# Kernel tuning notes

Hardware: AMD Instinct MI355X
Metric: run time of the kernel (lower is better)

Reference implementation:

```python
import jax, jax.numpy as jnp
import numpy as np
from jax import lax

SIGMA = 0.66  # e2cnn PointwiseAvgPoolAntialiased sigma -> 5x5 gaussian, stride 2, pad 2

def _conv(x, w, pad):
    return lax.conv_general_dilated(x, w, (1, 1), [(pad, pad), (pad, pad)],
                                    dimension_numbers=('NCHW', 'OIHW', 'NCHW'))

def _inner_bn(x, gamma, beta, fsize, eps=1e-5):
    # e2cnn InnerBatchNorm: stats shared across the fsize channels of each field
    B, C, H, W = x.shape
    F = C // fsize
    xr = x.reshape(B, F, fsize, H, W)
    m = xr.mean(axis=(0, 2, 3, 4), keepdims=True)
    v = xr.var(axis=(0, 2, 3, 4), keepdims=True)
    xr = (xr - m) * lax.rsqrt(v + eps)
    xr = xr * gamma.reshape(1, F, 1, 1, 1) + beta.reshape(1, F, 1, 1, 1)
    return xr.reshape(B, C, H, W)

def _gauss_pool(x):
    # antialiased avg-pool: depthwise 5x5 gaussian blur, stride 2, pad 2
    C = x.shape[1]
    r = jnp.arange(5.0) - 2.0
    k1 = jnp.exp(-r ** 2 / (2.0 * SIGMA ** 2))
    k2 = k1[:, None] * k1[None, :]
    k2 = (k2 / k2.sum()).astype(x.dtype)
    k = jnp.broadcast_to(k2, (C, 1, 5, 5))
    return lax.conv_general_dilated(x, k, (2, 2), [(2, 2), (2, 2)],
                                    feature_group_count=C,
                                    dimension_numbers=('NCHW', 'OIHW', 'NCHW'))

def _roi_align(feat, boxes, bidx, out=7, scale=0.25, ratio=2):
    # torchvision RoIAlign, aligned=True, sampling_ratio=2
    B, C, H, W = feat.shape
    Nb = boxes.shape[0]
    x1 = boxes[:, 0] * scale - 0.5
    y1 = boxes[:, 1] * scale - 0.5
    x2 = boxes[:, 2] * scale - 0.5
    y2 = boxes[:, 3] * scale - 0.5
    bw = (x2 - x1) / out
    bh = (y2 - y1) / out
    g = (jnp.arange(out * ratio, dtype=feat.dtype) + 0.5) / ratio  # [P] in bin units
    ys = y1[:, None] + bh[:, None] * g[None, :]  # [N,P]
    xs = x1[:, None] + bw[:, None] * g[None, :]
    vy = (ys >= -1.0) & (ys <= H)
    vx = (xs >= -1.0) & (xs <= W)
    y = jnp.clip(ys, 0.0, H - 1)
    x = jnp.clip(xs, 0.0, W - 1)
    y0f = jnp.floor(y); x0f = jnp.floor(x)
    y0 = y0f.astype(jnp.int32); x0 = x0f.astype(jnp.int32)
    yp = jnp.minimum(y0 + 1, H - 1); xp = jnp.minimum(x0 + 1, W - 1)
    ly = y - y0f; lx = x - x0f; hy = 1.0 - ly; hx = 1.0 - lx
    fp = feat.transpose(0, 2, 3, 1)  # [B,H,W,C]
    b3 = bidx[:, None, None]
    def gat(yi, xi):
        return fp[b3, yi[:, :, None], xi[:, None, :]]  # [N,P,P,C]
    val = (gat(y0, x0) * (hy[:, :, None] * hx[:, None, :])[..., None]
         + gat(y0, xp) * (hy[:, :, None] * lx[:, None, :])[..., None]
         + gat(yp, x0) * (ly[:, :, None] * hx[:, None, :])[..., None]
         + gat(yp, xp) * (ly[:, :, None] * lx[:, None, :])[..., None])
    val = val * (vy[:, :, None] & vx[:, None, :])[..., None].astype(val.dtype)
    val = val.reshape(Nb, out, ratio, out, ratio, C).mean(axis=(2, 4))
    return val.transpose(0, 3, 1, 2)  # [N,C,7,7]

def _gat_layer(x, src, dst, W, a_s, a_d, bias, heads, oc, concat, Nn):
    # PyG GATConv (eval mode: no dropout), negative_slope=0.2, self-loops in src/dst
    h = (x @ W.T).reshape(Nn, heads, oc)
    es = (h * a_s[None]).sum(-1)  # [N,H]
    ed = (h * a_d[None]).sum(-1)
    e = jax.nn.leaky_relu(es[src] + ed[dst], 0.2)  # [E,H]
    m = jax.ops.segment_max(e, dst, num_segments=Nn)
    e = jnp.exp(e - m[dst])
    den = jax.ops.segment_sum(e, dst, num_segments=Nn)
    alpha = e / (den[dst] + 1e-16)
    out = jax.ops.segment_sum(h[src] * alpha[..., None], dst, num_segments=Nn)
    out = out.reshape(Nn, heads * oc) if concat else out.mean(axis=1)
    return out + bias

def reference(images, boxes, box_batch_idx, edge_index,
              w_conv1, g1, b1, w_conv2, g2, b2, w_conv3, g3, b3,
              w_mlp1, b_mlp1, w_mlp2, b_mlp2,
              w_gat1, asrc1, adst1, bias1, w_gat2, asrc2, adst2, bias2,
              w_obj, b_obj, w_rel, b_rel):
    x = jax.nn.relu(_inner_bn(_conv(images, w_conv1, 1), g1, b1, 8))
    x = _gauss_pool(x)
    x = jax.nn.relu(_inner_bn(_conv(x, w_conv2, 1), g2, b2, 8))
    x = _gauss_pool(x)
    x = jax.nn.relu(_inner_bn(_conv(x, w_conv3, 0), g3, b3, 1))  # [B,64,56,56]
    roi = _roi_align(x, boxes, box_batch_idx)  # [N,64,7,7]
    Nn = roi.shape[0]
    r = roi.reshape(Nn, -1)
    h = jax.nn.relu(r @ w_mlp1.T + b_mlp1)
    h = jax.nn.relu(h @ w_mlp2.T + b_mlp2)
    loop = jnp.arange(Nn, dtype=edge_index.dtype)
    src = jnp.concatenate([edge_index[0], loop])
    dst = jnp.concatenate([edge_index[1], loop])
    h = _gat_layer(h, src, dst, w_gat1, asrc1, adst1, bias1, 4, 256, True, Nn)
    h = _gat_layer(h, src, dst, w_gat2, asrc2, adst2, bias2, 1, 256, False, Nn)
    obj_logits = h @ w_obj.T + b_obj
    ef = jnp.concatenate([h[edge_index[0]], h[edge_index[1]]], axis=1)
    rel_logits = ef @ w_rel.T + b_rel
    return obj_logits, rel_logits

def setup_inputs() -> dict:
    key = jax.random.key(0)
    ks = jax.random.split(key, 32)
    B, H, W = 4, 224, 224
    Nb, E, GH = 4096, 65536, 256
    images = jax.random.normal(ks[0], (B, 3, H, W), dtype=jnp.float32)
    x1 = jax.random.uniform(ks[1], (Nb,)) * 160.0
    y1 = jax.random.uniform(ks[2], (Nb,)) * 160.0
    bw = 16.0 + jax.random.uniform(ks[3], (Nb,)) * 48.0
    bh = 16.0 + jax.random.uniform(ks[4], (Nb,)) * 48.0
    boxes = jnp.stack([x1, y1, x1 + bw, y1 + bh], axis=1)
    box_batch_idx = jnp.sort(jax.random.randint(ks[5], (Nb,), 0, B, dtype=jnp.int32))
    edge_index = jax.random.randint(ks[6], (2, E), 0, Nb, dtype=jnp.int32)
    s = 0.02
    n = lambda k, shp: jax.random.normal(k, shp, dtype=jnp.float32) * s
    return {
        'images': images, 'boxes': boxes, 'box_batch_idx': box_batch_idx, 'edge_index': edge_index,
        'w_conv1': n(ks[7], (128, 3, 3, 3)), 'g1': jnp.ones((16,)), 'b1': jnp.zeros((16,)),
        'w_conv2': n(ks[8], (256, 128, 3, 3)), 'g2': jnp.ones((32,)), 'b2': jnp.zeros((32,)),
        'w_conv3': n(ks[9], (64, 256, 1, 1)), 'g3': jnp.ones((64,)), 'b3': jnp.zeros((64,)),
        'w_mlp1': n(ks[10], (GH, 64 * 7 * 7)), 'b_mlp1': jnp.zeros((GH,)),
        'w_mlp2': n(ks[11], (GH, GH)), 'b_mlp2': jnp.zeros((GH,)),
        'w_gat1': n(ks[12], (4 * GH, GH)), 'asrc1': n(ks[13], (4, GH)), 'adst1': n(ks[14], (4, GH)), 'bias1': jnp.zeros((4 * GH,)),
        'w_gat2': n(ks[15], (GH, 4 * GH)), 'asrc2': n(ks[16], (1, GH)), 'adst2': n(ks[17], (1, GH)), 'bias2': jnp.zeros((GH,)),
        'w_obj': n(ks[18], (151, GH)), 'b_obj': jnp.zeros((151,)),
        'w_rel': n(ks[19], (51, 2 * GH)), 'b_rel': jnp.zeros((51,)),
    }
```

## Files before the change

kernel.cpp:

```cpp
#include <hip/hip_runtime.h>
#include <hip/hip_bf16.h>
#include <cmath>

constexpr long Y1_F    = 0;
constexpr long Y3N_F   = 0;
constexpr long WM2B_F  = 0;
constexpr long WG1B_F  = 65536;
constexpr long WG2B_F  = 589824;
constexpr long ROI_F   = 12845056;
constexpr long Y2BF_F  = 12845056;
constexpr long WT2_F   = 16056320;
constexpr long O1_F    = 12845056;
constexpr long HG2_F   = 17039360;
constexpr long ES2_F   = 18087936;
constexpr long ED2_F   = 18092032;
constexpr long O2_F    = 18096128;
constexpr long Y2_F    = 25690112;
constexpr long HG1_F   = 25690112;
constexpr long ES1_F   = 29884416;
constexpr long ED1_F   = 29900800;
constexpr long Y4N_F   = 32112640;
constexpr long H1_F    = 32112640;
constexpr long H2_F    = 33161216;
constexpr long Y5N_F   = 35323904;
constexpr long STATS_F = 36126720;
constexpr long CNT_F   = 36127232;
constexpr long POS_F   = 36131328;
constexpr long OFF_F   = 36135424;
constexpr long EID_F   = 36139528;
constexpr long Y5T_F   = 36209160;
constexpr long WP_F    = 37011976;
constexpr long P1_F    = 37814792;
constexpr long P2_F    = 38023688;

struct GaussW { float w[25]; };

typedef __attribute__((ext_vector_type(8))) short bf16x8;
typedef __attribute__((ext_vector_type(4))) float f32x4;

static __device__ __forceinline__ unsigned short f2bf(float f) {
    unsigned int u = __float_as_uint(f);
    unsigned int r = (u + 0x7fffu + ((u >> 16) & 1u)) >> 16;
    return (unsigned short)r;
}

__global__ __launch_bounds__(256) void conv1_kernel(const float* __restrict__ img,
    const float* __restrict__ w, float* __restrict__ out) {
    int pb  = blockIdx.x % 196;
    int ocg = (blockIdx.x / 196) % 16;
    int b   = blockIdx.x / (196 * 16);
    int pix = pb * 256 + threadIdx.x;
    int y = pix / 224, x = pix % 224;
    const float* ib = img + (long)b * 3 * 50176;
    float in[27];
#pragma unroll
    for (int c = 0; c < 3; ++c)
#pragma unroll
        for (int dy = 0; dy < 3; ++dy) {
            int yy = y + dy - 1;
            bool oky = (unsigned)yy < 224u;
#pragma unroll
            for (int dx = 0; dx < 3; ++dx) {
                int xx = x + dx - 1;
                bool ok = oky && ((unsigned)xx < 224u);
                in[(c * 3 + dy) * 3 + dx] = ok ? ib[(c * 224 + yy) * 224 + xx] : 0.f;
            }
        }
    const float* wb = w + ocg * 8 * 27;
    float* ob = out + ((long)(b * 128 + ocg * 8)) * 50176 + pix;
#pragma unroll
    for (int o = 0; o < 8; ++o) {
        float a = 0.f;
#pragma unroll
        for (int j = 0; j < 27; ++j) a += in[j] * wb[o * 27 + j];
        ob[(long)o * 50176] = a;
    }
}

__global__ __launch_bounds__(256) void bn_stats_kernel(const float* __restrict__ x,
    double* __restrict__ stats, int C, int HW, int fs, int B) {
    int g = blockIdx.y;
    int fsHW = fs * HW;
    double s = 0.0, ss = 0.0;
    for (int b = 0; b < B; ++b) {
        const float* xb = x + ((long)b * C + (long)g * fs) * HW;
        for (int r = blockIdx.x * 256 + threadIdx.x; r < fsHW; r += gridDim.x * 256) {
            float v = xb[r];
            s += v; ss += (double)v * v;
        }
    }
    __shared__ double sh[512];
    sh[threadIdx.x] = s; sh[256 + threadIdx.x] = ss;
    __syncthreads();
    for (int st = 128; st > 0; st >>= 1) {
        if (threadIdx.x < st) {
            sh[threadIdx.x] += sh[threadIdx.x + st];
            sh[256 + threadIdx.x] += sh[256 + threadIdx.x + st];
        }
        __syncthreads();
    }
    if (threadIdx.x == 0) {
        atomicAdd(&stats[g * 2], sh[0]);
        atomicAdd(&stats[g * 2 + 1], sh[256]);
    }
}

__global__ __launch_bounds__(256) void gauss_pool_kernel(const float* __restrict__ in,
    float* __restrict__ out, const double* __restrict__ stats,
    const float* __restrict__ gamma, const float* __restrict__ beta,
    int C, int Hin, int Hout, int bpc, int fsLog, double invCnt, GaussW gw) {
    int pb = blockIdx.x % bpc;
    int c  = (blockIdx.x / bpc) % C;
    int b  = blockIdx.x / (bpc * C);
    int p  = pb * 256 + threadIdx.x;
    int HoW = Hout * Hout;
    if (p >= HoW) return;
    int oy = p / Hout, ox = p % Hout;
    int g = c >> fsLog;
    double sm = stats[g * 2], sq = stats[g * 2 + 1];
    double mean = sm * invCnt;
    double var  = sq * invCnt - mean * mean;
    float rs = rsqrtf((float)var + 1e-5f);
    float sc = gamma[g] * rs;
    float sh = beta[g] - (float)mean * sc;
    const float* ib = in + ((long)b * C + c) * Hin * Hin;
    float acc = 0.f;
#pragma unroll
    for (int dy = 0; dy < 5; ++dy) {
        int yy = 2 * oy + dy - 2;
        if ((unsigned)yy >= (unsigned)Hin) continue;
#pragma unroll
        for (int dx = 0; dx < 5; ++dx) {
            int xx = 2 * ox + dx - 2;
            if ((unsigned)xx >= (unsigned)Hin) continue;
            float v = fmaxf(ib[yy * Hin + xx] * sc + sh, 0.f);
            acc += v * gw.w[dy * 5 + dx];
        }
    }
    out[((long)b * C + c) * HoW + p] = acc;
}

__global__ __launch_bounds__(256) void nchw2nhwc_bf16(const float* __restrict__ in,
    unsigned short* __restrict__ out) {
    __shared__ float tile[128][65];
    int blk = blockIdx.x;
    int b = blk / 196, p0 = (blk % 196) * 64;
    int t = threadIdx.x;
#pragma unroll 4
    for (int i = 0; i < 32; ++i) {
        int idx = i * 256 + t; int c = idx >> 6; int p = idx & 63;
        tile[c][p] = in[((long)(b * 128 + c)) * 12544 + p0 + p];
    }
    __syncthreads();
#pragma unroll 4
    for (int i = 0; i < 32; ++i) {
        int idx = i * 256 + t; int p = idx >> 7; int c = idx & 127;
        out[((long)(b * 12544) + p0 + p) * 128 + c] = f2bf(tile[c][p]);
    }
}

__global__ __launch_bounds__(256) void wt2_kernel(const float* __restrict__ w,
    unsigned short* __restrict__ out) {
    int i = blockIdx.x * 256 + threadIdx.x;
    int o = i / 1152, k = i % 1152;
    int dydx = k >> 7, c = k & 127;
    out[i] = f2bf(w[(o * 128 + c) * 9 + dydx]);
}

__global__ __launch_bounds__(256) void castbf_kernel(const float* __restrict__ src,
    unsigned short* __restrict__ dst, int n) {
    int i = blockIdx.x * 256 + threadIdx.x;
    if (i < n) dst[i] = f2bf(src[i]);
}

__global__ __launch_bounds__(256) void conv2_mfma(
    const unsigned short* __restrict__ X,
    const unsigned short* __restrict__ Wt,
    float* __restrict__ out) {
    __shared__ __align__(16) short As[4096];
    __shared__ __align__(16) short Bs[4096];
    const int t = threadIdx.x;
    const int m0 = blockIdx.x * 128;
    const int n0 = blockIdx.y * 128;
    const int b  = m0 / 12544;
    const int pb = m0 % 12544;

    const int rA0 = t >> 2, rA1 = 64 + (t >> 2), cs = t & 3;
    const int p0 = pb + rA0, p1 = pb + rA1;
    const int y0 = p0 / 112, x0 = p0 % 112;
    const int y1 = p1 / 112, x1 = p1 % 112;
    short* aw0 = &As[rA0 * 32 + ((cs ^ ((rA0 >> 1) & 3)) * 8)];
    short* aw1 = &As[rA1 * 32 + ((cs ^ ((rA1 >> 1) & 3)) * 8)];
    short* bw0 = &Bs[rA0 * 32 + ((cs ^ ((rA0 >> 1) & 3)) * 8)];
    short* bw1 = &Bs[rA1 * 32 + ((cs ^ ((rA1 >> 1) & 3)) * 8)];
    const unsigned short* a0p = X + ((long)b * 12544 + p0) * 128 + cs * 8;
    const unsigned short* a1p = X + ((long)b * 12544 + p1) * 128 + cs * 8;
    const unsigned short* b0p = Wt + (long)(n0 + rA0) * 1152 + cs * 8;
    const unsigned short* b1p = Wt + (long)(n0 + rA1) * 1152 + cs * 8;

    const int lane = t & 63, wid = t >> 6;
    const int wr = wid >> 1, wc = wid & 1;
    const int fr = lane & 15, fc = lane >> 4;
    int ra[4], rb[4];
#pragma unroll
    for (int i = 0; i < 4; ++i) {
        int r = wr * 64 + i * 16 + fr;
        ra[i] = r * 32 + ((fc ^ ((r >> 1) & 3)) * 8);
        int rn = wc * 64 + i * 16 + fr;
        rb[i] = rn * 32 + ((fc ^ ((rn >> 1) & 3)) * 8);
    }
    f32x4 acc[4][4];
#pragma unroll
    for (int i = 0; i < 4; ++i)
#pragma unroll
        for (int j = 0; j < 4; ++j) acc[i][j] = (f32x4){0.f, 0.f, 0.f, 0.f};

    uint4 av0, av1, bv0, bv1;
    {
        int yy0 = y0 - 1, xx0 = x0 - 1, yy1 = y1 - 1, xx1 = x1 - 1;
        const int off = (-112 - 1) * 128;
        av0 = ((unsigned)yy0 < 112u && (unsigned)xx0 < 112u) ? *(const uint4*)(a0p + off) : make_uint4(0, 0, 0, 0);
        av1 = ((unsigned)yy1 < 112u && (unsigned)xx1 < 112u) ? *(const uint4*)(a1p + off) : make_uint4(0, 0, 0, 0);
        bv0 = *(const uint4*)(b0p);
        bv1 = *(const uint4*)(b1p);
    }
    for (int step = 0; step < 36; ++step) {
        __syncthreads();
        *(uint4*)aw0 = av0; *(uint4*)aw1 = av1;
        *(uint4*)bw0 = bv0; *(uint4*)bw1 = bv1;
        __syncthreads();
        if (step < 35) {
            int k0 = (step + 1) * 32;
            int dydx = k0 >> 7, coff = k0 & 127;
            int dy = dydx / 3 - 1, dx = dydx % 3 - 1;
            int off = (dy * 112 + dx) * 128 + coff;
            int yy0 = y0 + dy, xx0 = x0 + dx, yy1 = y1 + dy, xx1 = x1 + dx;
            av0 = ((unsigned)yy0 < 112u && (unsigned)xx0 < 112u) ? *(const uint4*)(a0p + off) : make_uint4(0, 0, 0, 0);
            av1 = ((unsigned)yy1 < 112u && (unsigned)xx1 < 112u) ? *(const uint4*)(a1p + off) : make_uint4(0, 0, 0, 0);
            bv0 = *(const uint4*)(b0p + k0);
            bv1 = *(const uint4*)(b1p + k0);
        }
        bf16x8 af[4], bfr[4];
#pragma unroll
        for (int i = 0; i < 4; ++i) {
            af[i]  = *(const bf16x8*)&As[ra[i]];
            bfr[i] = *(const bf16x8*)&Bs[rb[i]];
        }
#pragma unroll
        for (int i = 0; i < 4; ++i)
#pragma unroll
            for (int j = 0; j < 4; ++j)
                acc[i][j] = __builtin_amdgcn_mfma_f32_16x16x32_bf16(af[i], bfr[j], acc[i][j], 0, 0, 0);
    }
#pragma unroll
    for (int i = 0; i < 4; ++i) {
        int rbase = m0 + wr * 64 + i * 16 + fc * 4;
#pragma unroll
        for (int j = 0; j < 4; ++j) {
            int col = n0 + wc * 64 + j * 16 + fr;
#pragma unroll
            for (int r2 = 0; r2 < 4; ++r2)
                out[(long)(rbase + r2) * 256 + col] = acc[i][j][r2];
        }
    }
}

template <int RELU, int OUTBF>
__global__ __launch_bounds__(256) void bgemm_kernel(
    const unsigned short* __restrict__ A,
    const unsigned short* __restrict__ B,
    const float* __restrict__ bias,
    float* __restrict__ Cf, unsigned short* __restrict__ Cb,
    int M, int N, int K) {
    __shared__ __align__(16) short As[4096];
    __shared__ __align__(16) short Bs[4096];
    const int t = threadIdx.x;
    const int m0 = blockIdx.x * 128;
    const int n0 = blockIdx.y * 128;
    const int rA0 = t >> 2, rA1 = 64 + (t >> 2), cs = t & 3;
    short* aw0 = &As[rA0 * 32 + ((cs ^ ((rA0 >> 1) & 3)) * 8)];
    short* aw1 = &As[rA1 * 32 + ((cs ^ ((rA1 >> 1) & 3)) * 8)];
    short* bw0 = &Bs[rA0 * 32 + ((cs ^ ((rA0 >> 1) & 3)) * 8)];
    short* bw1 = &Bs[rA1 * 32 + ((cs ^ ((rA1 >> 1) & 3)) * 8)];
    const unsigned short* a0p = A + (long)(m0 + rA0) * K + cs * 8;
    const unsigned short* a1p = A + (long)(m0 + rA1) * K + cs * 8;
    const unsigned short* b0p = B + (long)(n0 + rA0) * K + cs * 8;
    const unsigned short* b1p = B + (long)(n0 + rA1) * K + cs * 8;

    const int lane = t & 63, wid = t >> 6;
    const int wr = wid >> 1, wc = wid & 1;
    const int fr = lane & 15, fc = lane >> 4;
    int ra[4], rb[4];
#pragma unroll
    for (int i = 0; i < 4; ++i) {
        int r = wr * 64 + i * 16 + fr;
        ra[i] = r * 32 + ((fc ^ ((r >> 1) & 3)) * 8);
        int rn = wc * 64 + i * 16 + fr;
        rb[i] = rn * 32 + ((fc ^ ((rn >> 1) & 3)) * 8);
    }
    f32x4 acc[4][4];
#pragma unroll
    for (int i = 0; i < 4; ++i)
#pragma unroll
        for (int j = 0; j < 4; ++j) acc[i][j] = (f32x4){0.f, 0.f, 0.f, 0.f};

    uint4 av0 = *(const uint4*)(a0p);
    uint4 av1 = *(const uint4*)(a1p);
    uint4 bv0 = *(const uint4*)(b0p);
    uint4 bv1 = *(const uint4*)(b1p);
    const int steps = K >> 5;
    for (int step = 0; step < steps; ++step) {
        __syncthreads();
        *(uint4*)aw0 = av0; *(uint4*)aw1 = av1;
        *(uint4*)bw0 = bv0; *(uint4*)bw1 = bv1;
        __syncthreads();
        if (step < steps - 1) {
            int k0 = (step + 1) * 32;
            av0 = *(const uint4*)(a0p + k0);
            av1 = *(const uint4*)(a1p + k0);
            bv0 = *(const uint4*)(b0p + k0);
            bv1 = *(const uint4*)(b1p + k0);
        }
        bf16x8 af[4], bfr[4];
#pragma unroll
        for (int i = 0; i < 4; ++i) {
            af[i]  = *(const bf16x8*)&As[ra[i]];
            bfr[i] = *(const bf16x8*)&Bs[rb[i]];
        }
#pragma unroll
        for (int i = 0; i < 4; ++i)
#pragma unroll
            for (int j = 0; j < 4; ++j)
                acc[i][j] = __builtin_amdgcn_mfma_f32_16x16x32_bf16(af[i], bfr[j], acc[i][j], 0, 0, 0);
    }
#pragma unroll
    for (int i = 0; i < 4; ++i) {
        int rbase = m0 + wr * 64 + i * 16 + fc * 4;
#pragma unroll
        for (int j = 0; j < 4; ++j) {
            int col = n0 + wc * 64 + j * 16 + fr;
            float bv = bias ? bias[col] : 0.f;
#pragma unroll
            for (int r2 = 0; r2 < 4; ++r2) {
                float v = acc[i][j][r2] + bv;
                if (RELU) v = fmaxf(v, 0.f);
                if (OUTBF) Cb[(long)(rbase + r2) * N + col] = f2bf(v);
                else       Cf[(long)(rbase + r2) * N + col] = v;
            }
        }
    }
}

__global__ __launch_bounds__(256) void bn_stats2_nhwc(const float* __restrict__ x,
    double* __restrict__ stats) {
    int t = threadIdx.x;
    long base = (long)blockIdx.x * 64 * 256;
    double s = 0.0, ss = 0.0;
    for (int p = 0; p < 64; ++p) {
        float v = x[base + p * 256 + t];
        s += v; ss += (double)v * v;
    }
    __shared__ double sh[512];
    sh[t] = s; sh[256 + t] = ss;
    __syncthreads();
    if (t < 32) {
        double gs = 0.0, gss = 0.0;
#pragma unroll
        for (int j = 0; j < 8; ++j) { gs += sh[8 * t + j]; gss += sh[256 + 8 * t + j]; }
        atomicAdd(&stats[t * 2], gs);
        atomicAdd(&stats[t * 2 + 1], gss);
    }
}

__global__ __launch_bounds__(256) void gauss_pool2_nhwc(const float* __restrict__ in,
    float* __restrict__ out, const double* __restrict__ stats,
    const float* __restrict__ gamma, const float* __restrict__ beta, GaussW gw) {
    int t = threadIdx.x;
    int g = t >> 3;
    double mean = stats[g * 2] * (1.0 / 401408.0);
    double var  = stats[g * 2 + 1] * (1.0 / 401408.0) - mean * mean;
    float rs = rsqrtf((float)var + 1e-5f);
    float sc = gamma[g] * rs;
    float shf = beta[g] - (float)mean * sc;
    int op = blockIdx.x;
    int b = op / 3136, r = op % 3136;
    int oy = r / 56, ox = r % 56;
    float acc = 0.f;
#pragma unroll
    for (int dy = 0; dy < 5; ++dy) {
        int yy = 2 * oy + dy - 2;
        if ((unsigned)yy >= 112u) continue;
#pragma unroll
        for (int dx = 0; dx < 5; ++dx) {
            int xx = 2 * ox + dx - 2;
            if ((unsigned)xx >= 112u) continue;
            float v = in[(((long)b * 12544) + yy * 112 + xx) * 256 + t];
            v = fmaxf(v * sc + shf, 0.f);
            acc += v * gw.w[dy * 5 + dx];
        }
    }
    out[(long)op * 256 + t] = acc;
}

__global__ __launch_bounds__(256) void bn_stats3_nhwc(const float* __restrict__ x,
    double* __restrict__ stats) {
    int t = threadIdx.x, c = t & 63, pr = t >> 6;
    long base = (long)blockIdx.x * 256 * 64;
    double s = 0.0, ss = 0.0;
    for (int p = pr; p < 256; p += 4) {
        float v = x[base + p * 64 + c];
        s += v; ss += (double)v * v;
    }
    __shared__ double sh[512];
    sh[t] = s; sh[256 + t] = ss;
    __syncthreads();
    if (t < 64) {
        double gs  = sh[t] + sh[64 + t] + sh[128 + t] + sh[192 + t];
        double gss = sh[256 + t] + sh[320 + t] + sh[384 + t] + sh[448 + t];
        atomicAdd(&stats[t * 2], gs);
        atomicAdd(&stats[t * 2 + 1], gss);
    }
}

__global__ __launch_bounds__(256) void bnrelu3_nhwc(const float* __restrict__ in,
    float* __restrict__ out, const double* __restrict__ stats,
    const float* __restrict__ gamma, const float* __restrict__ beta) {
    int i = blockIdx.x * 256 + threadIdx.x;
    int c = i & 63;
    double mean = stats[c * 2] * (1.0 / 12544.0);
    double var  = stats[c * 2 + 1] * (1.0 / 12544.0) - mean * mean;
    float rs = rsqrtf((float)var + 1e-5f);
    float sc = gamma[c] * rs;
    float sh = beta[c] - (float)mean * sc;
    out[i] = fmaxf(in[i] * sc + sh, 0.f);
}

__global__ __launch_bounds__(256) void wperm_kernel(const float* __restrict__ w,
    unsigned short* __restrict__ wp) {
    int gi = blockIdx.x * 256 + threadIdx.x;
    int o = gi / 3136, k = gi % 3136;
    int c = k & 63, p = k >> 6;
    wp[gi] = f2bf(w[(long)o * 3136 + c * 49 + p]);
}

__global__ __launch_bounds__(256) void roi_kernel(const float* __restrict__ fp,
    const float* __restrict__ boxes, const int* __restrict__ bidx,
    unsigned short* __restrict__ roi) {
    int gi = blockIdx.x * 256 + threadIdx.x;
    int c = gi & 63;
    int rest = gi >> 6;
    int p = rest % 49;
    int nb = rest / 49;
    int oy = p / 7, ox = p % 7;
    int b = bidx[nb];
    float x1 = boxes[nb * 4 + 0] * 0.25f - 0.5f;
    float y1 = boxes[nb * 4 + 1] * 0.25f - 0.5f;
    float x2 = boxes[nb * 4 + 2] * 0.25f - 0.5f;
    float y2 = boxes[nb * 4 + 3] * 0.25f - 0.5f;
    float bw = (x2 - x1) / 7.0f;
    float bh = (y2 - y1) / 7.0f;
    const float* fb = fp + (long)b * 3136 * 64;
    float acc = 0.f;
#pragma unroll
    for (int iy = 0; iy < 2; ++iy) {
        float gy = ((float)(oy * 2 + iy) + 0.5f) / 2.0f;
        float ys = y1 + bh * gy;
        bool vy = (ys >= -1.0f) && (ys <= 56.0f);
        float yc = fminf(fmaxf(ys, 0.f), 55.f);
        float y0f = floorf(yc);
        int y0 = (int)y0f;
        int yp = min(y0 + 1, 55);
        float ly = yc - y0f, hy = 1.f - ly;
#pragma unroll
        for (int ix = 0; ix < 2; ++ix) {
            float gx = ((float)(ox * 2 + ix) + 0.5f) / 2.0f;
            float xs = x1 + bw * gx;
            bool vx = (xs >= -1.0f) && (xs <= 56.0f);
            float xc = fminf(fmaxf(xs, 0.f), 55.f);
            float x0f = floorf(xc);
            int x0 = (int)x0f;
            int xp = min(x0 + 1, 55);
            float lx = xc - x0f, hx = 1.f - lx;
            float v00 = fb[(y0 * 56 + x0) * 64 + c];
            float v01 = fb[(y0 * 56 + xp) * 64 + c];
            float v10 = fb[(yp * 56 + x0) * 64 + c];
            float v11 = fb[(yp * 56 + xp) * 64 + c];
            float v = v00 * (hy * hx) + v01 * (hy * lx) + v10 * (ly * hx) + v11 * (ly * lx);
            acc += (vy && vx) ? v : 0.f;
        }
    }
    roi[(long)rest * 64 + c] = f2bf(acc * 0.25f);
}

__global__ __launch_bounds__(256) void gemm_kernel(const float* __restrict__ A,
    const float* __restrict__ W, const float* __restrict__ bias,
    float* __restrict__ C, int M, int N, int K, int ldw, int relu) {
    __shared__ float As[16][68];
    __shared__ float Ws[16][68];
    const int t = threadIdx.x;
    const int m0 = blockIdx.y * 64, n0 = blockIdx.x * 64;
    const int tx = t & 15, ty = t >> 4;
    const int lm = t >> 2, lk = (t & 3) * 4;
    float acc[4][4] = {};
    for (int k0 = 0; k0 < K; k0 += 16) {
        float4 av = *(const float4*)(A + (long)(m0 + lm) * K + (k0 + lk));
        float4 wv = make_float4(0.f, 0.f, 0.f, 0.f);
        if (n0 + lm < N) wv = *(const float4*)(W + (long)(n0 + lm) * ldw + (k0 + lk));
        As[lk + 0][lm] = av.x; As[lk + 1][lm] = av.y; As[lk + 2][lm] = av.z; As[lk + 3][lm] = av.w;
        Ws[lk + 0][lm] = wv.x; Ws[lk + 1][lm] = wv.y; Ws[lk + 2][lm] = wv.z; Ws[lk + 3][lm] = wv.w;
        __syncthreads();
#pragma unroll
        for (int k = 0; k < 16; ++k) {
            float4 a = *(const float4*)&As[k][ty * 4];
            float4 bv = *(const float4*)&Ws[k][tx * 4];
            acc[0][0] += a.x * bv.x; acc[0][1] += a.x * bv.y; acc[0][2] += a.x * bv.z; acc[0][3] += a.x * bv.w;
            acc[1][0] += a.y * bv.x; acc[1][1] += a.y * bv.y; acc[1][2] += a.y * bv.z; acc[1][3] += a.y * bv.w;
            acc[2][0] += a.z * bv.x; acc[2][1] += a.z * bv.y; acc[2][2] += a.z * bv.z; acc[2][3] += a.z * bv.w;
            acc[3][0] += a.w * bv.x; acc[3][1] += a.w * bv.y; acc[3][2] += a.w * bv.z; acc[3][3] += a.w * bv.w;
        }
        __syncthreads();
    }
#pragma unroll
    for (int i = 0; i < 4; ++i) {
        int m = m0 + ty * 4 + i;
#pragma unroll
        for (int j = 0; j < 4; ++j) {
            int n = n0 + tx * 4 + j;
            if (n < N) {
                float v = acc[i][j] + (bias ? bias[n] : 0.f);
                if (relu) v = fmaxf(v, 0.f);
                C[(long)m * N + n] = v;
            }
        }
    }
}

__global__ __launch_bounds__(256) void attn_dots_kernel(const float* __restrict__ h,
    const float* __restrict__ a_s, const float* __restrict__ a_d,
    float* __restrict__ es, float* __restrict__ ed, int heads) {
    int wid = (blockIdx.x * 256 + threadIdx.x) >> 6;
    int lane = threadIdx.x & 63;
    int hd = wid % heads;
    float4 hv = *(const float4*)&h[(long)wid * 256 + lane * 4];
    float4 av = *(const float4*)&a_s[hd * 256 + lane * 4];
    float4 dv = *(const float4*)&a_d[hd * 256 + lane * 4];
    float ps = hv.x * av.x + hv.y * av.y + hv.z * av.z + hv.w * av.w;
    float pd = hv.x * dv.x + hv.y * dv.y + hv.z * dv.z + hv.w * dv.w;
    for (int o = 32; o > 0; o >>= 1) {
        ps += __shfl_down(ps, o, 64);
        pd += __shfl_down(pd, o, 64);
    }
    if (lane == 0) { es[wid] = ps; ed[wid] = pd; }
}

__global__ __launch_bounds__(256) void edge_count_kernel(const int* __restrict__ ei,
    int* __restrict__ cnt, int E, int tot) {
    int k = blockIdx.x * 256 + threadIdx.x;
    if (k >= tot) return;
    int d = (k < E) ? ei[E + k] : (k - E);
    atomicAdd(&cnt[d], 1);
}

__global__ __launch_bounds__(1024) void scan_kernel(const int* __restrict__ cnt,
    int* __restrict__ off) {
    __shared__ int sh[1024];
    int t = threadIdx.x;
    int base = t * 4;
    int c0 = cnt[base], c1 = cnt[base + 1], c2 = cnt[base + 2], c3 = cnt[base + 3];
    sh[t] = c0 + c1 + c2 + c3;
    __syncthreads();
    for (int d = 1; d < 1024; d <<= 1) {
        int v = (t >= d) ? sh[t - d] : 0;
        __syncthreads();
        sh[t] += v;
        __syncthreads();
    }
    int excl = (t == 0) ? 0 : sh[t - 1];
    off[base] = excl;
    off[base + 1] = excl + c0;
    off[base + 2] = excl + c0 + c1;
    off[base + 3] = excl + c0 + c1 + c2;
    if (t == 1023) off[4096] = sh[1023];
}

__global__ __launch_bounds__(256) void edge_scatter_kernel(const int* __restrict__ ei,
    const int* __restrict__ off, int* __restrict__ pos, int* __restrict__ eid,
    int E, int tot) {
    int k = blockIdx.x * 256 + threadIdx.x;
    if (k >= tot) return;
    int d = (k < E) ? ei[E + k] : (k - E);
    int p = atomicAdd(&pos[d], 1);
    eid[off[d] + p] = k;
}

template <int HEADS, int OUTBF>
__global__ __launch_bounds__(256) void gat_aggregate_kernel(const float* __restrict__ h,
    const float* __restrict__ es, const float* __restrict__ ed,
    const int* __restrict__ off, const int* __restrict__ eid,
    const int* __restrict__ ei, const float* __restrict__ bias,
    void* __restrict__ outp, int E) {
    int n = blockIdx.x;
    int t = threadIdx.x;
    int o0 = off[n];
    int deg = off[n + 1] - o0;
    if (deg > 1024) deg = 1024;
    __shared__ float ew[4096];
    __shared__ int   srcs[1024];
    __shared__ float mden[2 * HEADS];
    for (int i = t; i < deg; i += 256) {
        int k = eid[o0 + i];
        int s = (k < E) ? ei[k] : (k - E);
        srcs[i] = s;
#pragma unroll
        for (int hd = 0; hd < HEADS; ++hd) {
            float e = es[s * HEADS + hd] + ed[n * HEADS + hd];
            e = (e >= 0.f) ? e : 0.2f * e;
            ew[i * HEADS + hd] = e;
        }
    }
    __syncthreads();
    if (t < HEADS) {
        float m = -1e30f;
        for (int i = 0; i < deg; ++i) m = fmaxf(m, ew[i * HEADS + t]);
        float den = 0.f;
        for (int i = 0; i < deg; ++i) den += expf(ew[i * HEADS + t] - m);
        mden[t] = m;
        mden[HEADS + t] = den + 1e-16f;
    }
    __syncthreads();
    for (int idx = t; idx < deg * HEADS; idx += 256) {
        int hd = idx % HEADS;
        ew[idx] = expf(ew[idx] - mden[hd]) / mden[HEADS + hd];
    }
    __syncthreads();
    float acc[HEADS];
#pragma unroll
    for (int hd = 0; hd < HEADS; ++hd) acc[hd] = 0.f;
    for (int i = 0; i < deg; ++i) {
        int s = srcs[i];
        const float* hr = &h[(long)s * HEADS * 256];
#pragma unroll
        for (int hd = 0; hd < HEADS; ++hd)
            acc[hd] += ew[i * HEADS + hd] * hr[hd * 256 + t];
    }
#pragma unroll
    for (int hd = 0; hd < HEADS; ++hd) {
        float v = acc[hd] + bias[hd * 256 + t];
        long oi = ((long)n * HEADS + hd) * 256 + t;
        if (OUTBF) ((unsigned short*)outp)[oi] = f2bf(v);
        else       ((float*)outp)[oi] = v;
    }
}

__global__ __launch_bounds__(256) void rel_scatter_kernel(const float* __restrict__ P1,
    const float* __restrict__ P2, const float* __restrict__ brel,
    const int* __restrict__ ei, float* __restrict__ out, int E) {
    int gi = blockIdx.x * 256 + threadIdx.x;
    int o = gi & 63;
    int e = gi >> 6;
    if (o >= 51 || e >= E) return;
    int s = ei[e], d = ei[E + e];
    out[(long)e * 51 + o] = P1[(long)s * 51 + o] + P2[(long)d * 51 + o] + brel[o];
}

extern "C" void kernel_launch(void* const* d_in, const int* in_sizes, int n_in,
                              void* d_out, int out_size, void* d_ws, size_t ws_size,
                              hipStream_t stream) {
    const float* images = (const float*)d_in[0];
    const float* boxes  = (const float*)d_in[1];
    const int*   bidx   = (const int*)d_in[2];
    const int*   ei     = (const int*)d_in[3];
    const float* w1     = (const float*)d_in[4];
    const float* g1     = (const float*)d_in[5];
    const float* b1     = (const float*)d_in[6];
    const float* w2     = (const float*)d_in[7];
    const float* g2     = (const float*)d_in[8];
    const float* b2     = (const float*)d_in[9];
    const float* w3     = (const float*)d_in[10];
    const float* g3     = (const float*)d_in[11];
    const float* b3     = (const float*)d_in[12];
    const float* wm1    = (const float*)d_in[13];
    const float* bm1    = (const float*)d_in[14];
    const float* wm2    = (const float*)d_in[15];
    const float* bm2    = (const float*)d_in[16];
    const float* wg1    = (const float*)d_in[17];
    const float* as1    = (const float*)d_in[18];
    const float* ad1    = (const float*)d_in[19];
    const float* bias1  = (const float*)d_in[20];
    const float* wg2    = (const float*)d_in[21];
    const float* as2    = (const float*)d_in[22];
    const float* ad2    = (const float*)d_in[23];
    const float* bias2  = (const float*)d_in[24];
    const float* wobj   = (const float*)d_in[25];
    const float* bobj   = (const float*)d_in[26];
    const float* wrel   = (const float*)d_in[27];
    const float* brel   = (const float*)d_in[28];

    float* ws = (float*)d_ws;
    float* out = (float*)d_out;
    const int E = 65536, TOT = 69632;

    float*  Y1   = ws + Y1_F;
    float*  Y2   = ws + Y2_F;
    float*  Y3N  = ws + Y3N_F;
    float*  Y4N  = ws + Y4N_F;
    float*  Y5N  = ws + Y5N_F;
    float*  Y5T  = ws + Y5T_F;
    float*  HG1  = ws + HG1_F;
    float*  ES1  = ws + ES1_F;
    float*  ED1  = ws + ED1_F;
    float*  HG2  = ws + HG2_F;
    float*  ES2  = ws + ES2_F;
    float*  ED2  = ws + ED2_F;
    float*  O2   = ws + O2_F;
    float*  P1   = ws + P1_F;
    float*  P2   = ws + P2_F;
    unsigned short* Y2BF = (unsigned short*)(ws + Y2BF_F);
    unsigned short* WT2  = (unsigned short*)(ws + WT2_F);
    unsigned short* ROIb = (unsigned short*)(ws + ROI_F);
    unsigned short* WPb  = (unsigned short*)(ws + WP_F);
    unsigned short* H1b  = (unsigned short*)(ws + H1_F);
    unsigned short* H2b  = (unsigned short*)(ws + H2_F);
    unsigned short* O1b  = (unsigned short*)(ws + O1_F);
    unsigned short* WM2b = (unsigned short*)(ws + WM2B_F);
    unsigned short* WG1b = (unsigned short*)(ws + WG1B_F);
    unsigned short* WG2b = (unsigned short*)(ws + WG2B_F);
    double* SD  = (double*)(ws + STATS_F);
    int*    CNT = (int*)(ws + CNT_F);
    int*    POS = (int*)(ws + POS_F);
    int*    OFF = (int*)(ws + OFF_F);
    int*    EID = (int*)(ws + EID_F);

    GaussW gw;
    {
        float k1[5];
        float s2 = 2.0f * 0.66f * 0.66f;
        for (int i = 0; i < 5; ++i) {
            float r = (float)i - 2.0f;
            k1[i] = expf(-r * r / s2);
        }
        float tot = 0.f;
        for (int i = 0; i < 5; ++i)
            for (int j = 0; j < 5; ++j) { gw.w[i * 5 + j] = k1[i] * k1[j]; tot += gw.w[i * 5 + j]; }
        for (int i = 0; i < 25; ++i) gw.w[i] /= tot;
    }

    hipMemsetAsync((char*)d_ws + STATS_F * 4, 0, (512 + 4096 + 4096) * 4, stream);

    conv1_kernel<<<12544, 256, 0, stream>>>(images, w1, Y1);
    bn_stats_kernel<<<dim3(128, 16), 256, 0, stream>>>(Y1, SD, 128, 50176, 8, 4);
    gauss_pool_kernel<<<4 * 128 * 49, 256, 0, stream>>>(Y1, Y2, SD, g1, b1,
        128, 224, 112, 49, 3, 1.0 / 1605632.0, gw);
    nchw2nhwc_bf16<<<784, 256, 0, stream>>>(Y2, Y2BF);
    wt2_kernel<<<1152, 256, 0, stream>>>(w2, WT2);
    conv2_mfma<<<dim3(392, 2), 256, 0, stream>>>(Y2BF, WT2, Y3N);
    bn_stats2_nhwc<<<784, 256, 0, stream>>>(Y3N, SD + 32);
    gauss_pool2_nhwc<<<12544, 256, 0, stream>>>(Y3N, Y4N, SD + 32, g2, b2, gw);
    gemm_kernel<<<dim3(1, 196), 256, 0, stream>>>(Y4N, w3, nullptr, Y5N, 12544, 64, 256, 256, 0);
    bn_stats3_nhwc<<<49, 256, 0, stream>>>(Y5N, SD + 96);
    bnrelu3_nhwc<<<3136, 256, 0, stream>>>(Y5N, Y5T, SD + 96, g3, b3);
    wperm_kernel<<<3136, 256, 0, stream>>>(wm1, WPb);
    castbf_kernel<<<256, 256, 0, stream>>>(wm2, WM2b, 65536);
    castbf_kernel<<<1024, 256, 0, stream>>>(wg1, WG1b, 262144);
    castbf_kernel<<<1024, 256, 0, stream>>>(wg2, WG2b, 262144);
    roi_kernel<<<50176, 256, 0, stream>>>(Y5T, boxes, bidx, ROIb);
    bgemm_kernel<1, 1><<<dim3(32, 2), 256, 0, stream>>>(ROIb, WPb, bm1, nullptr, H1b, 4096, 256, 3136);
    bgemm_kernel<1, 1><<<dim3(32, 2), 256, 0, stream>>>(H1b, WM2b, bm2, nullptr, H2b, 4096, 256, 256);
    edge_count_kernel<<<272, 256, 0, stream>>>(ei, CNT, E, TOT);
    scan_kernel<<<1, 1024, 0, stream>>>(CNT, OFF);
    edge_scatter_kernel<<<272, 256, 0, stream>>>(ei, OFF, POS, EID, E, TOT);
    bgemm_kernel<0, 0><<<dim3(32, 8), 256, 0, stream>>>(H2b, WG1b, nullptr, HG1, nullptr, 4096, 1024, 256);
    attn_dots_kernel<<<4096, 256, 0, stream>>>(HG1, as1, ad1, ES1, ED1, 4);
    gat_aggregate_kernel<4, 1><<<4096, 256, 0, stream>>>(HG1, ES1, ED1, OFF, EID, ei, bias1, O1b, E);
    bgemm_kernel<0, 0><<<dim3(32, 2), 256, 0, stream>>>(O1b, WG2b, nullptr, HG2, nullptr, 4096, 256, 1024);
    attn_dots_kernel<<<1024, 256, 0, stream>>>(HG2, as2, ad2, ES2, ED2, 1);
    gat_aggregate_kernel<1, 0><<<4096, 256, 0, stream>>>(HG2, ES2, ED2, OFF, EID, ei, bias2, O2, E);
    gemm_kernel<<<dim3(3, 64), 256, 0, stream>>>(O2, wobj, bobj, out, 4096, 151, 256, 256, 0);
    gemm_kernel<<<dim3(1, 64), 256, 0, stream>>>(O2, wrel, nullptr, P1, 4096, 51, 256, 512, 0);
    gemm_kernel<<<dim3(1, 64), 256, 0, stream>>>(O2, wrel + 256, nullptr, P2, 4096, 51, 256, 512, 0);
    rel_scatter_kernel<<<16384, 256, 0, stream>>>(P1, P2, brel, ei, out + 618496, E);
}
```

Baseline: 801.4 us.

## Fuse BN1 stats into conv1 and make first gaussian pool separable

```diff
diff --git a/kernel.cpp b/kernel.cpp
--- a/kernel.cpp
+++ b/kernel.cpp
@@ -34,6 +34,7 @@
 constexpr long P2_F    = 38023688;
 
 struct GaussW { float w[25]; };
+struct K5     { float k[5]; };
 
 typedef __attribute__((ext_vector_type(8))) short bf16x8;
 typedef __attribute__((ext_vector_type(4))) float f32x4;
@@ -45,7 +46,7 @@
 }
 
 __global__ __launch_bounds__(256) void conv1_kernel(const float* __restrict__ img,
-    const float* __restrict__ w, float* __restrict__ out) {
+    const float* __restrict__ w, float* __restrict__ out, double* __restrict__ stats) {
     int pb  = blockIdx.x % 196;
     int ocg = (blockIdx.x / 196) % 16;
     int b   = blockIdx.x / (196 * 16);
@@ -68,76 +69,75 @@
         }
     const float* wb = w + ocg * 8 * 27;
     float* ob = out + ((long)(b * 128 + ocg * 8)) * 50176 + pix;
+    double s = 0.0, ss = 0.0;
 #pragma unroll
     for (int o = 0; o < 8; ++o) {
         float a = 0.f;
 #pragma unroll
         for (int j = 0; j < 27; ++j) a += in[j] * wb[o * 27 + j];
         ob[(long)o * 50176] = a;
-    }
-}
-
-__global__ __launch_bounds__(256) void bn_stats_kernel(const float* __restrict__ x,
-    double* __restrict__ stats, int C, int HW, int fs, int B) {
-    int g = blockIdx.y;
-    int fsHW = fs * HW;
-    double s = 0.0, ss = 0.0;
-    for (int b = 0; b < B; ++b) {
-        const float* xb = x + ((long)b * C + (long)g * fs) * HW;
-        for (int r = blockIdx.x * 256 + threadIdx.x; r < fsHW; r += gridDim.x * 256) {
-            float v = xb[r];
-            s += v; ss += (double)v * v;
-        }
-    }
-    __shared__ double sh[512];
-    sh[threadIdx.x] = s; sh[256 + threadIdx.x] = ss;
+        s += a; ss += (double)a * a;
+    }
+    __shared__ double sh2[512];
+    int t = threadIdx.x;
+    sh2[t] = s; sh2[256 + t] = ss;
     __syncthreads();
     for (int st = 128; st > 0; st >>= 1) {
-        if (threadIdx.x < st) {
-            sh[threadIdx.x] += sh[threadIdx.x + st];
-            sh[256 + threadIdx.x] += sh[256 + threadIdx.x + st];
-        }
-        __syncthreads();
-    }
-    if (threadIdx.x == 0) {
-        atomicAdd(&stats[g * 2], sh[0]);
-        atomicAdd(&stats[g * 2 + 1], sh[256]);
-    }
-}
-
-__global__ __launch_bounds__(256) void gauss_pool_kernel(const float* __restrict__ in,
+        if (t < st) {
+            sh2[t] += sh2[t + st];
+            sh2[256 + t] += sh2[256 + t + st];
+        }
+        __syncthreads();
+    }
+    if (t == 0) {
+        atomicAdd(&stats[ocg * 2], sh2[0]);
+        atomicAdd(&stats[ocg * 2 + 1], sh2[256]);
+    }
+}
+
+__global__ __launch_bounds__(256) void gauss_pool1_sep(const float* __restrict__ in,
     float* __restrict__ out, const double* __restrict__ stats,
-    const float* __restrict__ gamma, const float* __restrict__ beta,
-    int C, int Hin, int Hout, int bpc, int fsLog, double invCnt, GaussW gw) {
-    int pb = blockIdx.x % bpc;
-    int c  = (blockIdx.x / bpc) % C;
-    int b  = blockIdx.x / (bpc * C);
-    int p  = pb * 256 + threadIdx.x;
-    int HoW = Hout * Hout;
-    if (p >= HoW) return;
-    int oy = p / Hout, ox = p % Hout;
-    int g = c >> fsLog;
-    double sm = stats[g * 2], sq = stats[g * 2 + 1];
-    double mean = sm * invCnt;
-    double var  = sq * invCnt - mean * mean;
+    const float* __restrict__ gamma, const float* __restrict__ beta, K5 kk) {
+    __shared__ float hbuf[19 * 112];
+    int blk = blockIdx.x;
+    int tile = blk % 14;
+    int c = (blk / 14) % 128;
+    int b = blk / (14 * 128);
+    int t = threadIdx.x;
+    int g = c >> 3;
+    double mean = stats[g * 2] * (1.0 / 1605632.0);
+    double var  = stats[g * 2 + 1] * (1.0 / 1605632.0) - mean * mean;
     float rs = rsqrtf((float)var + 1e-5f);
     float sc = gamma[g] * rs;
     float sh = beta[g] - (float)mean * sc;
-    const float* ib = in + ((long)b * C + c) * Hin * Hin;
-    float acc = 0.f;
-#pragma unroll
-    for (int dy = 0; dy < 5; ++dy) {
-        int yy = 2 * oy + dy - 2;
-        if ((unsigned)yy >= (unsigned)Hin) continue;
-#pragma unroll
-        for (int dx = 0; dx < 5; ++dx) {
-            int xx = 2 * ox + dx - 2;
-            if ((unsigned)xx >= (unsigned)Hin) continue;
-            float v = fmaxf(ib[yy * Hin + xx] * sc + sh, 0.f);
-            acc += v * gw.w[dy * 5 + dx];
-        }
-    }
-    out[((long)b * C + c) * HoW + p] = acc;
+    const float* ib = in + ((long)(b * 128 + c)) * 50176;
+    int y0 = tile * 16 - 2;
+    for (int i = t; i < 19 * 112; i += 256) {
+        int yl = i / 112, ox = i % 112;
+        int yy = y0 + yl;
+        float acc = 0.f;
+        if ((unsigned)yy < 224u) {
+            const float* row = ib + yy * 224;
+            int xb = 2 * ox - 2;
+#pragma unroll
+            for (int dx = 0; dx < 5; ++dx) {
+                int xx = xb + dx;
+                if ((unsigned)xx < 224u)
+                    acc += kk.k[dx] * fmaxf(row[xx] * sc + sh, 0.f);
+            }
+        }
+        hbuf[i] = acc;
+    }
+    __syncthreads();
+    float* ob = out + ((long)(b * 128 + c)) * 12544 + (tile * 8) * 112;
+    for (int i = t; i < 8 * 112; i += 256) {
+        int oyl = i / 112, ox = i % 112;
+        float acc = 0.f;
+#pragma unroll
+        for (int dy = 0; dy < 5; ++dy)
+            acc += kk.k[dy] * hbuf[(2 * oyl + dy) * 112 + ox];
+        ob[oyl * 112 + ox] = acc;
+    }
 }
 
 __global__ __launch_bounds__(256) void nchw2nhwc_bf16(const float* __restrict__ in,
@@ -732,6 +732,7 @@
     int*    EID = (int*)(ws + EID_F);
 
     GaussW gw;
+    K5 k5;
     {
         float k1[5];
         float s2 = 2.0f * 0.66f * 0.66f;
@@ -743,14 +744,15 @@
         for (int i = 0; i < 5; ++i)
             for (int j = 0; j < 5; ++j) { gw.w[i * 5 + j] = k1[i] * k1[j]; tot += gw.w[i * 5 + j]; }
         for (int i = 0; i < 25; ++i) gw.w[i] /= tot;
+        float s1 = 0.f;
+        for (int i = 0; i < 5; ++i) s1 += k1[i];
+        for (int i = 0; i < 5; ++i) k5.k[i] = k1[i] / s1;
     }
 
     hipMemsetAsync((char*)d_ws + STATS_F * 4, 0, (512 + 4096 + 4096) * 4, stream);
 
-    conv1_kernel<<<12544, 256, 0, stream>>>(images, w1, Y1);
-    bn_stats_kernel<<<dim3(128, 16), 256, 0, stream>>>(Y1, SD, 128, 50176, 8, 4);
-    gauss_pool_kernel<<<4 * 128 * 49, 256, 0, stream>>>(Y1, Y2, SD, g1, b1,
-        128, 224, 112, 49, 3, 1.0 / 1605632.0, gw);
+    conv1_kernel<<<12544, 256, 0, stream>>>(images, w1, Y1, SD);
+    gauss_pool1_sep<<<4 * 128 * 14, 256, 0, stream>>>(Y1, Y2, SD, g1, b1, k5);
     nchw2nhwc_bf16<<<784, 256, 0, stream>>>(Y2, Y2BF);
     wt2_kernel<<<1152, 256, 0, stream>>>(w2, WT2);
     conv2_mfma<<<dim3(392, 2), 256, 0, stream>>>(Y2BF, WT2, Y3N);
```

Result: slower. 825.1 us (+3.0%).
